# Kernel optimization log

Hardware: AMD Instinct MI355X
Metric: run time of the kernel (lower is better)

The kernel has to match this reference:

```python
import math
import jax, jax.numpy as jnp
import numpy as np

LLM = 4096
QB = 512
SAM = 256
H = W = 64
OUT = 256
HEADS = 4
DH = SAM // HEADS
EPS = 1e-5


def _ln(x, g, b):
    mu = jnp.mean(x, axis=-1, keepdims=True)
    var = jnp.mean(jnp.square(x - mu), axis=-1, keepdims=True)
    return (x - mu) * jax.lax.rsqrt(var + EPS) * g + b


def _conv3x3(x, w):
    # x: (N,C,H,W), w: (O,I,3,3), padding=1
    return jax.lax.conv_general_dilated(
        x, w, window_strides=(1, 1), padding='SAME',
        dimension_numbers=('NCHW', 'OIHW', 'NCHW'))


def setup_inputs() -> dict:
    key = jax.random.key(0)
    ks = jax.random.split(key, 20)
    n = lambda k, sh, s: (jax.random.normal(k, sh, dtype=jnp.float32) * s)
    inp = {
        'image_embed': n(ks[0], (8, SAM, H, W), 1.0),
        'ref_vec': n(ks[1], (8, 32, LLM), 1.0),
        'querybook_slots': n(ks[2], (8, 32, QB), 1.0),
        # parameters (torch Linear layout: (out, in); conv: (O,I,kh,kw))
        'q_proj_w': n(ks[3], (HEADS * DH, LLM), 1.0 / math.sqrt(LLM)),
        'k_proj_w': n(ks[4], (HEADS * DH, SAM, 1, 1), 1.0 / math.sqrt(SAM)),
        'fuser_w1': n(ks[5], (HEADS, HEADS, 3, 3), 1.0 / math.sqrt(HEADS * 9)),
        'fuser_b1': n(ks[6], (HEADS,), 0.01),
        'fuser_w2': n(ks[7], (1, HEADS, 3, 3), 1.0 / math.sqrt(HEADS * 9)),
        'fuser_b2': jnp.full((1,), -1.8, dtype=jnp.float32),
        'qb_proj_w': n(ks[8], (LLM, QB), 1.0 / math.sqrt(QB)),
        'rf_ln_g': jnp.ones((2 * LLM,), jnp.float32),
        'rf_ln_b': jnp.zeros((2 * LLM,), jnp.float32),
        'rf_lin_w': n(ks[9], (LLM, 2 * LLM), 1.0 / math.sqrt(2 * LLM)),
        'rf_lin_b': n(ks[10], (LLM,), 0.01),
        'cf_ln_g': jnp.ones((LLM,), jnp.float32),
        'cf_ln_b': jnp.zeros((LLM,), jnp.float32),
        'cf_w1': n(ks[11], (LLM // 2, LLM), 1.0 / math.sqrt(LLM)),
        'cf_b1': n(ks[12], (LLM // 2,), 0.01),
        'cf_w2': n(ks[13], (1, LLM // 2), 1.0 / math.sqrt(LLM // 2)),
        'cf_b2': n(ks[14], (1,), 0.01),
    }
    return inp


def reference(image_embed, ref_vec, querybook_slots, q_proj_w, k_proj_w,
              fuser_w1, fuser_b1, fuser_w2, fuser_b2, qb_proj_w,
              rf_ln_g, rf_ln_b, rf_lin_w, rf_lin_b,
              cf_ln_g, cf_ln_b, cf_w1, cf_b1, cf_w2, cf_b2):
    B, C, h, w = image_embed.shape
    K = ref_vec.shape[1]
    # querybook projection + ref fuse
    qb = jnp.einsum('bkq,lq->bkl', querybook_slots, qb_proj_w)  # (B,K,LLM)
    cat = jnp.concatenate([ref_vec, qb], axis=-1)               # (B,K,2*LLM)
    fused = jax.nn.silu(jnp.einsum('bkc,lc->bkl', _ln(cat, rf_ln_g, rf_ln_b), rf_lin_w) + rf_lin_b)
    # per-slot query heads
    Q = jnp.einsum('bkl,ol->bko', fused, q_proj_w).reshape(B, K, HEADS, DH)
    # 1x1 conv key map -> (B,HEADS,DH,H,W)
    Kmap = jnp.einsum('bcxy,oc->boxy', image_embed, k_proj_w.reshape(HEADS * DH, SAM))
    Kmap = Kmap.reshape(B, HEADS, DH, h, w)
    # fused contraction over d_head (original materialized (B,K,HEADS,DH,H,W))
    logits_64_heads = jnp.einsum('bkhd,bhdxy->bkhxy', Q, Kmap) / math.sqrt(DH)
    x = logits_64_heads.reshape(B * K, HEADS, h, w)
    x = jax.nn.silu(_conv3x3(x, fuser_w1) + fuser_b1[None, :, None, None])
    logits_64 = _conv3x3(x, fuser_w2) + fuser_b2[None, :, None, None]  # (B*K,1,64,64)
    # bilinear upsample, align_corners=False (half-pixel centers)
    up = jax.image.resize(logits_64, (B * K, 1, OUT, OUT), method='bilinear')
    ref_logits_256 = up.reshape(B, K, OUT, OUT)
    # confidence head
    cfh = jax.nn.silu(jnp.einsum('bkl,ol->bko', _ln(fused, cf_ln_g, cf_ln_b), cf_w1) + cf_b1)
    conf_logits = (jnp.einsum('bko,lo->bkl', cfh, cf_w2) + cf_b2).squeeze(-1)  # (B,K)
    return ref_logits_256, conf_logits
```

## Files before the change

### kernel.cpp

```cpp
#include <hip/hip_runtime.h>

#define EPS 1e-5f

typedef __bf16 bf16_t;
typedef __bf16 bf16x8 __attribute__((ext_vector_type(8)));
typedef __bf16 bf16x4 __attribute__((ext_vector_type(4)));
typedef float f32x4 __attribute__((ext_vector_type(4)));

__device__ __forceinline__ float silu_f(float x) { return x / (1.f + __expf(-x)); }

__device__ __forceinline__ void gll16(const void* g, void* l) {
  __builtin_amdgcn_global_load_lds(
      (const __attribute__((address_space(1))) unsigned int*)g,
      (__attribute__((address_space(3))) unsigned int*)l, 16, 0, 0);
}

__device__ __forceinline__ float block_sum(float v, float* tmp) {
#pragma unroll
  for (int off = 32; off > 0; off >>= 1) v += __shfl_down(v, off);
  __syncthreads();
  if ((threadIdx.x & 63) == 0) tmp[threadIdx.x >> 6] = v;
  __syncthreads();
  return tmp[0] + tmp[1] + tmp[2] + tmp[3];
}

__global__ __launch_bounds__(1024) void gemm_gll(
    const bf16_t* __restrict__ A, const float* __restrict__ B,
    bf16_t* __restrict__ Cpart, int N, int K, int KS) {
  __shared__ bf16_t AsL[2][16384];
  __shared__ float BsL[2][8192];
  const int t = threadIdx.x;
  const int lane = t & 63;
  const int w = t >> 6;
  const int n0 = blockIdx.x * 128;
  const int kbeg = blockIdx.y * KS;
  const int nt = KS >> 6;

  const int arow0 = 16 * w + (lane >> 3);
  const int adch = (lane & 7) ^ (lane >> 3);
  const bf16_t* gA0 = A + (size_t)arow0 * K + kbeg + adch * 8;
  const bf16_t* gA1 = gA0 + (size_t)8 * K;
  const int brow0 = 8 * w + (lane >> 4);
  const int brow1 = brow0 + 4;
  const int bd0 = (lane & 15) ^ (brow0 & 15);
  const int bd1 = (lane & 15) ^ (brow1 & 15);
  const float* gB0 = B + (size_t)(n0 + brow0) * K + kbeg + bd0 * 4;
  const float* gB1 = B + (size_t)(n0 + brow1) * K + kbeg + bd1 * 4;

  f32x4 acc[4][2];
#pragma unroll
  for (int i = 0; i < 4; ++i)
#pragma unroll
    for (int j = 0; j < 2; ++j) acc[i][j] = f32x4{0.f, 0.f, 0.f, 0.f};

  const int wm = (w & 3) * 64;
  const int wn = (w >> 2) * 32;
  const int fr = lane & 15;
  const int kq = (lane >> 4) * 8;

  auto ISSUE = [&](int s, int p) {
    const int koff = s * 64;
    char* ab = (char*)&AsL[p][0] + 2 * w * 1024;
    char* bb = (char*)&BsL[p][0] + 2 * w * 1024;
    gll16(gA0 + koff, ab);
    gll16(gA1 + koff, ab + 1024);
    gll16(gB0 + koff, bb);
    gll16(gB1 + koff, bb + 1024);
  };

  auto COMPUTE = [&](int p) {
    const char* Ab = (const char*)&AsL[p][0];
    const char* Bb = (const char*)&BsL[p][0];
#pragma unroll
    for (int kk = 0; kk < 64; kk += 32) {
      const int col = kk + kq;
      bf16x8 af[4], bg[2];
#pragma unroll
      for (int i = 0; i < 4; ++i) {
        const int ra = wm + 16 * i + fr;
        const int sa = (col >> 3) ^ (ra & 7);
        af[i] = *(const bf16x8*)(Ab + ra * 128 + sa * 16);
      }
#pragma unroll
      for (int j = 0; j < 2; ++j) {
        const int rb = wn + 16 * j + fr;
        const int c0 = col >> 2;
        const int s0 = c0 ^ (rb & 15);
        const int s1 = (c0 + 1) ^ (rb & 15);
        f32x4 u0 = *(const f32x4*)(Bb + rb * 256 + s0 * 16);
        f32x4 u1 = *(const f32x4*)(Bb + rb * 256 + s1 * 16);
        bf16x8 bv;
        bv[0] = (bf16_t)u0[0]; bv[1] = (bf16_t)u0[1];
        bv[2] = (bf16_t)u0[2]; bv[3] = (bf16_t)u0[3];
        bv[4] = (bf16_t)u1[0]; bv[5] = (bf16_t)u1[1];
        bv[6] = (bf16_t)u1[2]; bv[7] = (bf16_t)u1[3];
        bg[j] = bv;
      }
#pragma unroll
      for (int i = 0; i < 4; ++i)
#pragma unroll
        for (int j = 0; j < 2; ++j)
          acc[i][j] = __builtin_amdgcn_mfma_f32_16x16x32_bf16(af[i], bg[j], acc[i][j], 0, 0, 0);
    }
  };

#define SB __builtin_amdgcn_sched_barrier(0);

  ISSUE(0, 0);
  if (nt > 1) ISSUE(1, 1);
  for (int s = 0; s < nt; ++s) {
    const int p = s & 1;
    if (s + 1 < nt) {
      asm volatile("s_waitcnt vmcnt(4)" ::: "memory");
    } else {
      asm volatile("s_waitcnt vmcnt(0)" ::: "memory");
    }
    SB __builtin_amdgcn_s_barrier(); SB
    COMPUTE(p);
    if (s + 2 < nt) {
      asm volatile("s_waitcnt lgkmcnt(0)" ::: "memory");
      SB __builtin_amdgcn_s_barrier(); SB
      ISSUE(s + 2, p);
    }
  }
#undef SB

  bf16_t* Cz = Cpart + (size_t)blockIdx.y * 256 * N;
  const int rh = (lane >> 4) * 4, col = lane & 15;
#pragma unroll
  for (int i = 0; i < 4; ++i)
#pragma unroll
    for (int j = 0; j < 2; ++j)
#pragma unroll
      for (int rr = 0; rr < 4; ++rr)
        Cz[(size_t)(wm + 16 * i + rh + rr) * N + n0 + wn + 16 * j + col] =
            (bf16_t)acc[i][j][rr];
}

__global__ __launch_bounds__(1024) void gemm_wide_s(
    const float* __restrict__ A, const float* __restrict__ B,
    bf16_t* __restrict__ Cpart, int N, int K, int KS) {
  __shared__ bf16_t As[256][72];
  __shared__ bf16_t Bs[128][72];
  const int t = threadIdx.x;
  const int lane = t & 63;
  const int w = t >> 6;
  const int n0 = blockIdx.x * 128;
  const int kbeg = blockIdx.y * KS;
  const int nt = KS >> 6;
  const int ar = t >> 2, ac = (t & 3) * 16;
  const int br = t >> 3, bc = (t & 7) * 8;
  const float* Ap = A + (size_t)ar * K + kbeg + ac;
  const float* Bp = B + (size_t)(n0 + br) * K + kbeg + bc;

  f32x4 acc[4][2];
#pragma unroll
  for (int i = 0; i < 4; ++i)
#pragma unroll
    for (int j = 0; j < 2; ++j) acc[i][j] = f32x4{0.f, 0.f, 0.f, 0.f};

  const int wm = (w & 3) * 64;
  const int wn = (w >> 2) * 32;
  const int fr = lane & 15;
  const int kq = (lane >> 4) * 8;

  for (int s = 0; s < nt; ++s) {
    float4 av[4], bv[2];
#pragma unroll
    for (int i = 0; i < 4; ++i) av[i] = *(const float4*)(Ap + s * 64 + 4 * i);
#pragma unroll
    for (int i = 0; i < 2; ++i) bv[i] = *(const float4*)(Bp + s * 64 + 4 * i);
    __syncthreads();
    {
      bf16x8 wa0, wa1, wb;
      wa0[0] = (bf16_t)av[0].x; wa0[1] = (bf16_t)av[0].y; wa0[2] = (bf16_t)av[0].z; wa0[3] = (bf16_t)av[0].w;
      wa0[4] = (bf16_t)av[1].x; wa0[5] = (bf16_t)av[1].y; wa0[6] = (bf16_t)av[1].z; wa0[7] = (bf16_t)av[1].w;
      wa1[0] = (bf16_t)av[2].x; wa1[1] = (bf16_t)av[2].y; wa1[2] = (bf16_t)av[2].z; wa1[3] = (bf16_t)av[2].w;
      wa1[4] = (bf16_t)av[3].x; wa1[5] = (bf16_t)av[3].y; wa1[6] = (bf16_t)av[3].z; wa1[7] = (bf16_t)av[3].w;
      wb[0] = (bf16_t)bv[0].x; wb[1] = (bf16_t)bv[0].y; wb[2] = (bf16_t)bv[0].z; wb[3] = (bf16_t)bv[0].w;
      wb[4] = (bf16_t)bv[1].x; wb[5] = (bf16_t)bv[1].y; wb[6] = (bf16_t)bv[1].z; wb[7] = (bf16_t)bv[1].w;
      *(bf16x8*)&As[ar][ac] = wa0;
      *(bf16x8*)&As[ar][ac + 8] = wa1;
      *(bf16x8*)&Bs[br][bc] = wb;
    }
    __syncthreads();
#pragma unroll
    for (int kk = 0; kk < 64; kk += 32) {
      bf16x8 af[4], bg[2];
#pragma unroll
      for (int i = 0; i < 4; ++i)
        af[i] = *(const bf16x8*)&As[wm + 16 * i + fr][kk + kq];
#pragma unroll
      for (int j = 0; j < 2; ++j)
        bg[j] = *(const bf16x8*)&Bs[wn + 16 * j + fr][kk + kq];
#pragma unroll
      for (int i = 0; i < 4; ++i)
#pragma unroll
        for (int j = 0; j < 2; ++j)
          acc[i][j] = __builtin_amdgcn_mfma_f32_16x16x32_bf16(af[i], bg[j], acc[i][j], 0, 0, 0);
    }
    __syncthreads();
  }

  bf16_t* Cz = Cpart + (size_t)blockIdx.y * 256 * N;
  const int rh = (lane >> 4) * 4, col = lane & 15;
#pragma unroll
  for (int i = 0; i < 4; ++i)
#pragma unroll
    for (int j = 0; j < 2; ++j)
#pragma unroll
      for (int rr = 0; rr < 4; ++rr)
        Cz[(size_t)(wm + 16 * i + rh + rr) * N + n0 + wn + 16 * j + col] =
            (bf16_t)acc[i][j][rr];
}

__global__ __launch_bounds__(256) void gemm_small(
    const bf16_t* __restrict__ A16, const float* __restrict__ B32, float* __restrict__ Cv,
    int M, int N, int K, int KS, int S) {
  __shared__ bf16_t As[64][72];
  __shared__ bf16_t Bs[64][72];
  const int t = threadIdx.x;
  const int lane = t & 63;
  const int w = t >> 6;
  const int s = blockIdx.z;
  const int n0 = blockIdx.x * 64;
  const int m0 = blockIdx.y * 64;
  const int kbeg = s * KS;

  f32x4 acc[2][2];
#pragma unroll
  for (int i = 0; i < 2; ++i)
#pragma unroll
    for (int j = 0; j < 2; ++j) acc[i][j] = f32x4{0.f, 0.f, 0.f, 0.f};

  const int wm = (w & 1) * 32, wn = (w >> 1) * 32;
  const int fr = lane & 15;
  const int kq = (lane >> 4) * 8;

  for (int k0 = kbeg; k0 < kbeg + KS; k0 += 64) {
    bf16x8 a8[2];
    float4 b4[4];
    {
      const int rr = t >> 2, c8 = (t & 3) * 8;
#pragma unroll
      for (int i = 0; i < 2; ++i)
        a8[i] = *(const bf16x8*)(A16 + (size_t)(m0 + rr) * K + k0 + c8 + 32 * i);
    }
    {
      const int rr = t >> 4, c4 = (t & 15) * 4;
#pragma unroll
      for (int i = 0; i < 4; ++i)
        b4[i] = *(const float4*)(B32 + (size_t)(n0 + rr + 16 * i) * K + k0 + c4);
    }
    __syncthreads();
    {
      const int rr = t >> 2, c8 = (t & 3) * 8;
#pragma unroll
      for (int i = 0; i < 2; ++i) *(bf16x8*)&As[rr][c8 + 32 * i] = a8[i];
    }
    {
      const int rr = t >> 4, c4 = (t & 15) * 4;
#pragma unroll
      for (int i = 0; i < 4; ++i) {
        bf16x4 v = {(bf16_t)b4[i].x, (bf16_t)b4[i].y, (bf16_t)b4[i].z, (bf16_t)b4[i].w};
        *(bf16x4*)&Bs[rr + 16 * i][c4] = v;
      }
    }
    __syncthreads();
#pragma unroll
    for (int kk = 0; kk < 64; kk += 32) {
      bf16x8 af[2], bg[2];
#pragma unroll
      for (int i = 0; i < 2; ++i) {
        af[i] = *(const bf16x8*)&As[wm + 16 * i + fr][kk + kq];
        bg[i] = *(const bf16x8*)&Bs[wn + 16 * i + fr][kk + kq];
      }
#pragma unroll
      for (int i = 0; i < 2; ++i)
#pragma unroll
        for (int j = 0; j < 2; ++j)
          acc[i][j] = __builtin_amdgcn_mfma_f32_16x16x32_bf16(af[i], bg[j], acc[i][j], 0, 0, 0);
    }
    __syncthreads();
  }

  const int rh = (lane >> 4) * 4;
  const int col = lane & 15;
#pragma unroll
  for (int i = 0; i < 2; ++i)
#pragma unroll
    for (int j = 0; j < 2; ++j)
#pragma unroll
      for (int rr = 0; rr < 4; ++rr)
        Cv[(size_t)s * M * N + (size_t)(m0 + wm + 16 * i + rh + rr) * N + n0 + wn + 16 * j + col] =
            acc[i][j][rr];
}

__global__ __launch_bounds__(512) void gemm_attn(
    const float* __restrict__ A, const float* __restrict__ B, bf16_t* __restrict__ C) {
  __shared__ bf16_t As[128][72];
  __shared__ bf16_t Bs[64][72];
  const int t = threadIdx.x;
  const int lane = t & 63;
  const int w = t >> 6;
  const int b = blockIdx.y;
  const int n0 = blockIdx.x * 64;
  const float* Ab = A + (size_t)b * 32768;
  const float* Bb = B + (size_t)b * 1048576;

  f32x4 acc[2][2];
#pragma unroll
  for (int i = 0; i < 2; ++i)
#pragma unroll
    for (int j = 0; j < 2; ++j) acc[i][j] = f32x4{0.f, 0.f, 0.f, 0.f};

  const int wm = (w & 3) * 32;
  const int wn = (w >> 2) * 32;
  const int fr = lane & 15;
  const int kq = (lane >> 4) * 8;

  for (int k0 = 0; k0 < 256; k0 += 64) {
    const int r = t >> 2, c4 = (t & 3) * 16;
    float4 a4[4];
#pragma unroll
    for (int i = 0; i < 4; ++i)
      a4[i] = *(const float4*)(Ab + (size_t)r * 256 + k0 + c4 + 4 * i);
    const int kr = t >> 3, nc = (t & 7) * 8;
    float4 b4[2];
#pragma unroll
    for (int i = 0; i < 2; ++i)
      b4[i] = *(const float4*)(Bb + (size_t)(k0 + kr) * 4096 + n0 + nc + 4 * i);
    __syncthreads();
#pragma unroll
    for (int i = 0; i < 4; ++i) {
      bf16x4 v = {(bf16_t)a4[i].x, (bf16_t)a4[i].y, (bf16_t)a4[i].z, (bf16_t)a4[i].w};
      *(bf16x4*)&As[r][c4 + 4 * i] = v;
    }
#pragma unroll
    for (int i = 0; i < 2; ++i) {
      Bs[nc + 4 * i + 0][kr] = (bf16_t)b4[i].x;
      Bs[nc + 4 * i + 1][kr] = (bf16_t)b4[i].y;
      Bs[nc + 4 * i + 2][kr] = (bf16_t)b4[i].z;
      Bs[nc + 4 * i + 3][kr] = (bf16_t)b4[i].w;
    }
    __syncthreads();
#pragma unroll
    for (int kk = 0; kk < 64; kk += 32) {
      bf16x8 af[2], bg[2];
#pragma unroll
      for (int i = 0; i < 2; ++i) {
        af[i] = *(const bf16x8*)&As[wm + 16 * i + fr][kk + kq];
        bg[i] = *(const bf16x8*)&Bs[wn + 16 * i + fr][kk + kq];
      }
#pragma unroll
      for (int i = 0; i < 2; ++i)
#pragma unroll
        for (int j = 0; j < 2; ++j)
          acc[i][j] = __builtin_amdgcn_mfma_f32_16x16x32_bf16(af[i], bg[j], acc[i][j], 0, 0, 0);
    }
    __syncthreads();
  }

  bf16_t* Cb = C + (size_t)b * 524288;
  const int rh = (lane >> 4) * 4, col = lane & 15;
#pragma unroll
  for (int i = 0; i < 2; ++i)
#pragma unroll
    for (int j = 0; j < 2; ++j)
#pragma unroll
      for (int rr = 0; rr < 4; ++rr)
        Cb[(size_t)(wm + 16 * i + rh + rr) * 4096 + n0 + wn + 16 * j + col] =
            (bf16_t)acc[i][j][rr];
}

template <int SILU_, int BIAS_>
__global__ __launch_bounds__(256) void reduce_b(
    const bf16_t* __restrict__ part, int S, long slice,
    const float* __restrict__ bias, float scale,
    float* __restrict__ outF, bf16_t* __restrict__ outB,
    long nmask, long total8) {
  long i8 = (long)blockIdx.x * 256 + threadIdx.x;
  if (i8 >= total8) return;
  long i = i8 * 8;
  float a[8] = {0.f, 0.f, 0.f, 0.f, 0.f, 0.f, 0.f, 0.f};
  for (int s = 0; s < S; ++s) {
    bf16x8 v = *(const bf16x8*)(part + (size_t)s * slice + i);
#pragma unroll
    for (int j = 0; j < 8; ++j) a[j] += (float)v[j];
  }
#pragma unroll
  for (int j = 0; j < 8; ++j) a[j] *= scale;
  if (BIAS_) {
    const float* bb = bias + (i & nmask);
#pragma unroll
    for (int j = 0; j < 8; ++j) a[j] += bb[j];
  }
  if (SILU_) {
#pragma unroll
    for (int j = 0; j < 8; ++j) a[j] = silu_f(a[j]);
  }
  if (outF) {
    float4 o0 = {a[0], a[1], a[2], a[3]}, o1 = {a[4], a[5], a[6], a[7]};
    *(float4*)(outF + i) = o0;
    *(float4*)(outF + i + 4) = o1;
  }
  if (outB) {
    bf16x8 o;
#pragma unroll
    for (int j = 0; j < 8; ++j) o[j] = (bf16_t)a[j];
    *(bf16x8*)(outB + i) = o;
  }
}

__global__ __launch_bounds__(256) void ln_fuse(
    const float* __restrict__ refv, const bf16_t* __restrict__ partQ, int S,
    const float* __restrict__ g, const float* __restrict__ bta, bf16_t* __restrict__ Y) {
  __shared__ float tmp[4];
  const int row = blockIdx.x;
  const int t = threadIdx.x;
  const long i0 = t * 16;
  float q[16];
#pragma unroll
  for (int j = 0; j < 16; ++j) q[j] = 0.f;
  for (int s = 0; s < S; ++s) {
    const bf16_t* p = partQ + (size_t)s * 1048576 + (size_t)row * 4096 + i0;
    bf16x8 v0 = *(const bf16x8*)(p);
    bf16x8 v1 = *(const bf16x8*)(p + 8);
#pragma unroll
    for (int j = 0; j < 8; ++j) { q[j] += (float)v0[j]; q[8 + j] += (float)v1[j]; }
  }
  const float* xr = refv + (size_t)row * 4096 + i0;
  float r[16];
#pragma unroll
  for (int j = 0; j < 4; ++j) {
    float4 v = *(const float4*)(xr + 4 * j);
    r[4 * j] = v.x; r[4 * j + 1] = v.y; r[4 * j + 2] = v.z; r[4 * j + 3] = v.w;
  }
  float s1 = 0.f, s2 = 0.f;
#pragma unroll
  for (int j = 0; j < 16; ++j) { s1 += r[j] + q[j]; s2 += r[j] * r[j] + q[j] * q[j]; }
  s1 = block_sum(s1, tmp);
  s2 = block_sum(s2, tmp);
  const float mu = s1 / 8192.f;
  const float inv = rsqrtf(s2 / 8192.f - mu * mu + EPS);
  bf16_t* y = Y + (size_t)row * 8192;
  bf16x8 o0, o1;
#pragma unroll
  for (int j = 0; j < 8; ++j) {
    o0[j] = (bf16_t)((r[j] - mu) * inv * g[i0 + j] + bta[i0 + j]);
    o1[j] = (bf16_t)((r[8 + j] - mu) * inv * g[i0 + 8 + j] + bta[i0 + 8 + j]);
  }
  *(bf16x8*)(y + i0) = o0;
  *(bf16x8*)(y + i0 + 8) = o1;
#pragma unroll
  for (int j = 0; j < 8; ++j) {
    o0[j] = (bf16_t)((q[j] - mu) * inv * g[4096 + i0 + j] + bta[4096 + i0 + j]);
    o1[j] = (bf16_t)((q[8 + j] - mu) * inv * g[4096 + i0 + 8 + j] + bta[4096 + i0 + 8 + j]);
  }
  *(bf16x8*)(y + 4096 + i0) = o0;
  *(bf16x8*)(y + 4096 + i0 + 8) = o1;
}

__global__ __launch_bounds__(256) void ln_rows(
    const float* __restrict__ X1, int L1,
    const float* __restrict__ g, const float* __restrict__ bta, bf16_t* __restrict__ Y) {
  __shared__ float tmp[4];
  const int row = blockIdx.x;
  const float* x1 = X1 + (size_t)row * L1;
  float s = 0.f, ss = 0.f;
  for (int i = threadIdx.x * 4; i < L1; i += 1024) {
    float4 v = *(const float4*)(x1 + i);
    s += v.x + v.y + v.z + v.w;
    ss += v.x * v.x + v.y * v.y + v.z * v.z + v.w * v.w;
  }
  s = block_sum(s, tmp);
  ss = block_sum(ss, tmp);
  const float mu = s / (float)L1;
  const float inv = rsqrtf(ss / (float)L1 - mu * mu + EPS);
  bf16_t* y = Y + (size_t)row * L1;
  for (int i = threadIdx.x * 4; i < L1; i += 1024) {
    float4 v = *(const float4*)(x1 + i);
    float4 gv = *(const float4*)(g + i);
    float4 bv = *(const float4*)(bta + i);
    bf16x4 o = {(bf16_t)((v.x - mu) * inv * gv.x + bv.x),
                (bf16_t)((v.y - mu) * inv * gv.y + bv.y),
                (bf16_t)((v.z - mu) * inv * gv.z + bv.z),
                (bf16_t)((v.w - mu) * inv * gv.w + bv.w)};
    *(bf16x4*)(y + i) = o;
  }
}

__global__ __launch_bounds__(256) void qw_fuse(
    const float* __restrict__ part8, const float* __restrict__ kW, float* __restrict__ QW) {
  __shared__ float q[256];
  const int bk = blockIdx.x;
  const int c = threadIdx.x;
  float sq = 0.f;
#pragma unroll
  for (int s = 0; s < 8; ++s) sq += part8[(size_t)s * 65536 + (size_t)bk * 256 + c];
  q[c] = 0.125f * sq;
  __syncthreads();
#pragma unroll
  for (int h = 0; h < 4; ++h) {
    float s = 0.f;
#pragma unroll 8
    for (int d = 0; d < 64; ++d)
      s += q[(h << 6) + d] * kW[(size_t)(((h << 6) + d) << 8) + c];
    QW[((size_t)(bk * 4 + h) << 8) + c] = s;
  }
}

__global__ __launch_bounds__(256) void conv_fused(
    const bf16_t* __restrict__ X, const float* __restrict__ W1,
    const float* __restrict__ B1, const float* __restrict__ W2,
    const float* __restrict__ B2, float* __restrict__ O) {
  __shared__ bf16_t lg[16384];
  __shared__ bf16_t mid[16384];
  __shared__ float lg64[4096];
  __shared__ float wsh[180];
  const int t = threadIdx.x;
  const size_t base = (size_t)blockIdx.x * 16384;
#pragma unroll
  for (int i = 0; i < 8; ++i) {
    int o = (i * 256 + t) * 8;
    *(bf16x8*)&lg[o] = *(const bf16x8*)(X + base + o);
  }
  if (t < 144) wsh[t] = W1[t];
  else if (t < 180) wsh[t] = W2[t - 144];
  __syncthreads();
  const int px0 = (t & 15) * 4, py0 = (t >> 4) * 4;
  {
    float acc1[4][16];
#pragma unroll
    for (int oc = 0; oc < 4; ++oc) {
      float bb = B1[oc];
#pragma unroll
      for (int p = 0; p < 16; ++p) acc1[oc][p] = bb;
    }
#pragma unroll
    for (int c = 0; c < 4; ++c) {
      float p[6][6];
#pragma unroll
      for (int yy = 0; yy < 6; ++yy) {
        int gy = py0 + yy - 1;
#pragma unroll
        for (int xx = 0; xx < 6; ++xx) {
          int gx = px0 + xx - 1;
          p[yy][xx] = ((unsigned)gy < 64u && (unsigned)gx < 64u)
                          ? (float)lg[c * 4096 + gy * 64 + gx] : 0.f;
        }
      }
#pragma unroll
      for (int oc = 0; oc < 4; ++oc) {
        float wr[9];
#pragma unroll
        for (int k = 0; k < 9; ++k) wr[k] = wsh[oc * 36 + c * 9 + k];
#pragma unroll
        for (int y = 0; y < 4; ++y)
#pragma unroll
          for (int x = 0; x < 4; ++x)
            acc1[oc][y * 4 + x] +=
                wr[0] * p[y][x] + wr[1] * p[y][x + 1] + wr[2] * p[y][x + 2]
              + wr[3] * p[y + 1][x] + wr[4] * p[y + 1][x + 1] + wr[5] * p[y + 1][x + 2]
              + wr[6] * p[y + 2][x] + wr[7] * p[y + 2][x + 1] + wr[8] * p[y + 2][x + 2];
      }
    }
#pragma unroll
    for (int oc = 0; oc < 4; ++oc)
#pragma unroll
      for (int y = 0; y < 4; ++y) {
        bf16x4 o;
#pragma unroll
        for (int x = 0; x < 4; ++x) o[x] = (bf16_t)silu_f(acc1[oc][y * 4 + x]);
        *(bf16x4*)&mid[oc * 4096 + (py0 + y) * 64 + px0] = o;
      }
  }
  __syncthreads();
  {
    float acc2[16];
    float bb = B2[0];
#pragma unroll
    for (int p = 0; p < 16; ++p) acc2[p] = bb;
#pragma unroll
    for (int c = 0; c < 4; ++c) {
      float p[6][6];
#pragma unroll
      for (int yy = 0; yy < 6; ++yy) {
        int gy = py0 + yy - 1;
#pragma unroll
        for (int xx = 0; xx < 6; ++xx) {
          int gx = px0 + xx - 1;
          p[yy][xx] = ((unsigned)gy < 64u && (unsigned)gx < 64u)
                          ? (float)mid[c * 4096 + gy * 64 + gx] : 0.f;
        }
      }
      float wr[9];
#pragma unroll
      for (int k = 0; k < 9; ++k) wr[k] = wsh[144 + c * 9 + k];
#pragma unroll
      for (int y = 0; y < 4; ++y)
#pragma unroll
        for (int x = 0; x < 4; ++x)
          acc2[y * 4 + x] +=
              wr[0] * p[y][x] + wr[1] * p[y][x + 1] + wr[2] * p[y][x + 2]
            + wr[3] * p[y + 1][x] + wr[4] * p[y + 1][x + 1] + wr[5] * p[y + 1][x + 2]
            + wr[6] * p[y + 2][x] + wr[7] * p[y + 2][x + 1] + wr[8] * p[y + 2][x + 2];
    }
#pragma unroll
    for (int y = 0; y < 4; ++y)
#pragma unroll
      for (int x = 0; x < 4; ++x) lg64[(py0 + y) * 64 + px0 + x] = acc2[y * 4 + x];
  }
  __syncthreads();
  float* Ob = O + (size_t)blockIdx.x * 65536;
  for (int rr = 0; rr < 64; ++rr) {
    int p4 = rr * 256 + t;
    int oy = p4 >> 6, ox0 = (p4 & 63) * 4;
    float sy = oy * 0.25f - 0.375f;
    int y0 = (int)floorf(sy);
    float wy = sy - (float)y0;
    int y1 = min(y0 + 1, 63); y0 = max(y0, 0);
    const float* r0 = &lg64[y0 * 64];
    const float* r1 = &lg64[y1 * 64];
    float4 o;
#pragma unroll
    for (int q = 0; q < 4; ++q) {
      int ox = ox0 + q;
      float sx = ox * 0.25f - 0.375f;
      int x0 = (int)floorf(sx);
      float wx = sx - (float)x0;
      int x1 = min(x0 + 1, 63); x0 = max(x0, 0);
      float v0 = r0[x0] + wx * (r0[x1] - r0[x0]);
      float v1 = r1[x0] + wx * (r1[x1] - r1[x0]);
      ((float*)&o)[q] = v0 + wy * (v1 - v0);
    }
    *(float4*)(Ob + oy * 256 + ox0) = o;
  }
}

__global__ __launch_bounds__(256) void conf_k(
    const float* __restrict__ cfh, const float* __restrict__ w2,
    const float* __restrict__ b2, float* __restrict__ out) {
  __shared__ float tmp[4];
  const int row = blockIdx.x;
  float s = 0.f;
  for (int i = threadIdx.x; i < 2048; i += 256)
    s += cfh[(size_t)row * 2048 + i] * w2[i];
  s = block_sum(s, tmp);
  if (threadIdx.x == 0) out[row] = s + b2[0];
}

extern "C" void kernel_launch(void* const* d_in, const int* in_sizes, int n_in,
                              void* d_out, int out_size, void* d_ws, size_t ws_size,
                              hipStream_t stream) {
  const float* img    = (const float*)d_in[0];
  const float* refv   = (const float*)d_in[1];
  const float* qs     = (const float*)d_in[2];
  const float* qpw    = (const float*)d_in[3];
  const float* kpw    = (const float*)d_in[4];
  const float* fw1    = (const float*)d_in[5];
  const float* fb1    = (const float*)d_in[6];
  const float* fw2    = (const float*)d_in[7];
  const float* fb2    = (const float*)d_in[8];
  const float* qbw    = (const float*)d_in[9];
  const float* rlg    = (const float*)d_in[10];
  const float* rlb    = (const float*)d_in[11];
  const float* rlw    = (const float*)d_in[12];
  const float* rlbias = (const float*)d_in[13];
  const float* clg    = (const float*)d_in[14];
  const float* clb    = (const float*)d_in[15];
  const float* cw1    = (const float*)d_in[16];
  const float* cb1    = (const float*)d_in[17];
  const float* cw2    = (const float*)d_in[18];
  const float* cb2    = (const float*)d_in[19];
  float* out = (float*)d_out;
  char* W = (char*)d_ws;

  bf16_t* partQ = (bf16_t*)(W + 0);
  bf16_t* partF = (bf16_t*)(W + 0);
  bf16_t* l64hb = (bf16_t*)(W + 0);
  bf16_t* partC = (bf16_t*)(W + 0);
  bf16_t* catln = (bf16_t*)(W + 16777216);
  float*  fus   = (float*)(W + 16777216);
  bf16_t* fusb  = (bf16_t*)(W + 20971520);
  bf16_t* lnf   = (bf16_t*)(W + 20971520);
  float*  part8 = (float*)(W + 23068672);
  float*  QW    = (float*)(W + 25165824);
  float*  cfh   = (float*)(W + 26214400);

  dim3 b256(256);

  gemm_wide_s<<<dim3(32, 8), dim3(1024), 0, stream>>>(qs, qbw, partQ, 4096, 512, 64);
  ln_fuse<<<dim3(256), b256, 0, stream>>>(refv, partQ, 8, rlg, rlb, catln);
  gemm_gll<<<dim3(32, 8), dim3(1024), 0, stream>>>(catln, rlw, partF, 4096, 8192, 1024);
  reduce_b<1, 1><<<dim3(512), b256, 0, stream>>>(
      partF, 8, 1048576L, rlbias, 1.f, fus, fusb, 4095L, 131072L);
  gemm_small<<<dim3(4, 4, 8), b256, 0, stream>>>(fusb, qpw, part8, 256, 256, 4096, 512, 8);
  qw_fuse<<<dim3(256), b256, 0, stream>>>(part8, kpw, QW);
  gemm_attn<<<dim3(64, 8), dim3(512), 0, stream>>>(QW, img, l64hb);
  conv_fused<<<dim3(256), b256, 0, stream>>>(l64hb, fw1, fb1, fw2, fb2, out);
  ln_rows<<<dim3(256), b256, 0, stream>>>(fus, 4096, clg, clb, lnf);
  gemm_gll<<<dim3(16, 8), dim3(1024), 0, stream>>>(lnf, cw1, partC, 2048, 4096, 512);
  reduce_b<1, 1><<<dim3(256), b256, 0, stream>>>(
      partC, 8, 524288L, cb1, 1.f, cfh, nullptr, 2047L, 65536L);
  conf_k<<<dim3(256), b256, 0, stream>>>(cfh, cw2, cb2, out + 16777216);
}
```

Before: 184.7 us.

## Fuse split-K reduction with LayerNorm and confidence head, widen conf GEMM split

The split-K reduction after the fusion linear now also computes the confidence-head LayerNorm, writing the bf16 fused and normalized rows in one kernel. This drops the fp32 intermediate and the separate ln_rows pass. The confidence GEMM's split-K factor goes from 8 to 16 for more blocks. Its reduction, bias, SiLU and final dot product are fused into one kernel, removing two launches and the fp32 cfh buffer. The cost is reading twice as many partial sums in the last reduction.

```diff
diff --git a/kernel.cpp b/kernel.cpp
--- a/kernel.cpp
+++ b/kernel.cpp
@@ -373,43 +373,49 @@
             (bf16_t)acc[i][j][rr];
 }
 
-template <int SILU_, int BIAS_>
-__global__ __launch_bounds__(256) void reduce_b(
-    const bf16_t* __restrict__ part, int S, long slice,
-    const float* __restrict__ bias, float scale,
-    float* __restrict__ outF, bf16_t* __restrict__ outB,
-    long nmask, long total8) {
-  long i8 = (long)blockIdx.x * 256 + threadIdx.x;
-  if (i8 >= total8) return;
-  long i = i8 * 8;
-  float a[8] = {0.f, 0.f, 0.f, 0.f, 0.f, 0.f, 0.f, 0.f};
+__global__ __launch_bounds__(256) void red_ln(
+    const bf16_t* __restrict__ partF, int S,
+    const float* __restrict__ bias,
+    const float* __restrict__ g, const float* __restrict__ bta,
+    bf16_t* __restrict__ fusb, bf16_t* __restrict__ lnf) {
+  __shared__ float tmp[4];
+  const int row = blockIdx.x;
+  const int t = threadIdx.x;
+  const long i0 = t * 16;
+  float a[16];
+#pragma unroll
+  for (int j = 0; j < 16; ++j) a[j] = 0.f;
   for (int s = 0; s < S; ++s) {
-    bf16x8 v = *(const bf16x8*)(part + (size_t)s * slice + i);
-#pragma unroll
-    for (int j = 0; j < 8; ++j) a[j] += (float)v[j];
-  }
-#pragma unroll
-  for (int j = 0; j < 8; ++j) a[j] *= scale;
-  if (BIAS_) {
-    const float* bb = bias + (i & nmask);
-#pragma unroll
-    for (int j = 0; j < 8; ++j) a[j] += bb[j];
-  }
-  if (SILU_) {
-#pragma unroll
-    for (int j = 0; j < 8; ++j) a[j] = silu_f(a[j]);
-  }
-  if (outF) {
-    float4 o0 = {a[0], a[1], a[2], a[3]}, o1 = {a[4], a[5], a[6], a[7]};
-    *(float4*)(outF + i) = o0;
-    *(float4*)(outF + i + 4) = o1;
-  }
-  if (outB) {
-    bf16x8 o;
-#pragma unroll
-    for (int j = 0; j < 8; ++j) o[j] = (bf16_t)a[j];
-    *(bf16x8*)(outB + i) = o;
-  }
+    const bf16_t* p = partF + (size_t)s * 1048576 + (size_t)row * 4096 + i0;
+    bf16x8 v0 = *(const bf16x8*)(p);
+    bf16x8 v1 = *(const bf16x8*)(p + 8);
+#pragma unroll
+    for (int j = 0; j < 8; ++j) { a[j] += (float)v0[j]; a[8 + j] += (float)v1[j]; }
+  }
+#pragma unroll
+  for (int j = 0; j < 16; ++j) a[j] = silu_f(a[j] + bias[i0 + j]);
+  {
+    bf16x8 o0, o1;
+#pragma unroll
+    for (int j = 0; j < 8; ++j) { o0[j] = (bf16_t)a[j]; o1[j] = (bf16_t)a[8 + j]; }
+    *(bf16x8*)(fusb + (size_t)row * 4096 + i0) = o0;
+    *(bf16x8*)(fusb + (size_t)row * 4096 + i0 + 8) = o1;
+  }
+  float s1 = 0.f, s2 = 0.f;
+#pragma unroll
+  for (int j = 0; j < 16; ++j) { s1 += a[j]; s2 += a[j] * a[j]; }
+  s1 = block_sum(s1, tmp);
+  s2 = block_sum(s2, tmp);
+  const float mu = s1 / 4096.f;
+  const float inv = rsqrtf(s2 / 4096.f - mu * mu + EPS);
+  bf16x8 o0, o1;
+#pragma unroll
+  for (int j = 0; j < 8; ++j) {
+    o0[j] = (bf16_t)((a[j] - mu) * inv * g[i0 + j] + bta[i0 + j]);
+    o1[j] = (bf16_t)((a[8 + j] - mu) * inv * g[i0 + 8 + j] + bta[i0 + 8 + j]);
+  }
+  *(bf16x8*)(lnf + (size_t)row * 4096 + i0) = o0;
+  *(bf16x8*)(lnf + (size_t)row * 4096 + i0 + 8) = o1;
 }
 
 __global__ __launch_bounds__(256) void ln_fuse(
@@ -459,35 +465,6 @@
   }
   *(bf16x8*)(y + 4096 + i0) = o0;
   *(bf16x8*)(y + 4096 + i0 + 8) = o1;
-}
-
-__global__ __launch_bounds__(256) void ln_rows(
-    const float* __restrict__ X1, int L1,
-    const float* __restrict__ g, const float* __restrict__ bta, bf16_t* __restrict__ Y) {
-  __shared__ float tmp[4];
-  const int row = blockIdx.x;
-  const float* x1 = X1 + (size_t)row * L1;
-  float s = 0.f, ss = 0.f;
-  for (int i = threadIdx.x * 4; i < L1; i += 1024) {
-    float4 v = *(const float4*)(x1 + i);
-    s += v.x + v.y + v.z + v.w;
-    ss += v.x * v.x + v.y * v.y + v.z * v.z + v.w * v.w;
-  }
-  s = block_sum(s, tmp);
-  ss = block_sum(ss, tmp);
-  const float mu = s / (float)L1;
-  const float inv = rsqrtf(ss / (float)L1 - mu * mu + EPS);
-  bf16_t* y = Y + (size_t)row * L1;
-  for (int i = threadIdx.x * 4; i < L1; i += 1024) {
-    float4 v = *(const float4*)(x1 + i);
-    float4 gv = *(const float4*)(g + i);
-    float4 bv = *(const float4*)(bta + i);
-    bf16x4 o = {(bf16_t)((v.x - mu) * inv * gv.x + bv.x),
-                (bf16_t)((v.y - mu) * inv * gv.y + bv.y),
-                (bf16_t)((v.z - mu) * inv * gv.z + bv.z),
-                (bf16_t)((v.w - mu) * inv * gv.w + bv.w)};
-    *(bf16x4*)(y + i) = o;
-  }
 }
 
 __global__ __launch_bounds__(256) void qw_fuse(
@@ -638,16 +615,27 @@
   }
 }
 
-__global__ __launch_bounds__(256) void conf_k(
-    const float* __restrict__ cfh, const float* __restrict__ w2,
+__global__ __launch_bounds__(256) void conf_fuse(
+    const bf16_t* __restrict__ partC, int S,
+    const float* __restrict__ cb1, const float* __restrict__ w2,
     const float* __restrict__ b2, float* __restrict__ out) {
   __shared__ float tmp[4];
   const int row = blockIdx.x;
-  float s = 0.f;
-  for (int i = threadIdx.x; i < 2048; i += 256)
-    s += cfh[(size_t)row * 2048 + i] * w2[i];
-  s = block_sum(s, tmp);
-  if (threadIdx.x == 0) out[row] = s + b2[0];
+  const int t = threadIdx.x;
+  const long i0 = t * 8;
+  float a[8];
+#pragma unroll
+  for (int j = 0; j < 8; ++j) a[j] = 0.f;
+  for (int s = 0; s < S; ++s) {
+    bf16x8 v = *(const bf16x8*)(partC + (size_t)s * 524288 + (size_t)row * 2048 + i0);
+#pragma unroll
+    for (int j = 0; j < 8; ++j) a[j] += (float)v[j];
+  }
+  float dot = 0.f;
+#pragma unroll
+  for (int j = 0; j < 8; ++j) dot += silu_f(a[j] + cb1[i0 + j]) * w2[i0 + j];
+  dot = block_sum(dot, tmp);
+  if (t == 0) out[row] = dot + b2[0];
 }
 
 extern "C" void kernel_launch(void* const* d_in, const int* in_sizes, int n_in,
@@ -681,27 +669,21 @@
   bf16_t* l64hb = (bf16_t*)(W + 0);
   bf16_t* partC = (bf16_t*)(W + 0);
   bf16_t* catln = (bf16_t*)(W + 16777216);
-  float*  fus   = (float*)(W + 16777216);
   bf16_t* fusb  = (bf16_t*)(W + 20971520);
-  bf16_t* lnf   = (bf16_t*)(W + 20971520);
-  float*  part8 = (float*)(W + 23068672);
-  float*  QW    = (float*)(W + 25165824);
-  float*  cfh   = (float*)(W + 26214400);
+  bf16_t* lnf   = (bf16_t*)(W + 23068672);
+  float*  part8 = (float*)(W + 25165824);
+  float*  QW    = (float*)(W + 27262976);
 
   dim3 b256(256);
 
   gemm_wide_s<<<dim3(32, 8), dim3(1024), 0, stream>>>(qs, qbw, partQ, 4096, 512, 64);
   ln_fuse<<<dim3(256), b256, 0, stream>>>(refv, partQ, 8, rlg, rlb, catln);
   gemm_gll<<<dim3(32, 8), dim3(1024), 0, stream>>>(catln, rlw, partF, 4096, 8192, 1024);
-  reduce_b<1, 1><<<dim3(512), b256, 0, stream>>>(
-      partF, 8, 1048576L, rlbias, 1.f, fus, fusb, 4095L, 131072L);
+  red_ln<<<dim3(256), b256, 0, stream>>>(partF, 8, rlbias, clg, clb, fusb, lnf);
   gemm_small<<<dim3(4, 4, 8), b256, 0, stream>>>(fusb, qpw, part8, 256, 256, 4096, 512, 8);
   qw_fuse<<<dim3(256), b256, 0, stream>>>(part8, kpw, QW);
   gemm_attn<<<dim3(64, 8), dim3(512), 0, stream>>>(QW, img, l64hb);
   conv_fused<<<dim3(256), b256, 0, stream>>>(l64hb, fw1, fb1, fw2, fb2, out);
-  ln_rows<<<dim3(256), b256, 0, stream>>>(fus, 4096, clg, clb, lnf);
-  gemm_gll<<<dim3(16, 8), dim3(1024), 0, stream>>>(lnf, cw1, partC, 2048, 4096, 512);
-  reduce_b<1, 1><<<dim3(256), b256, 0, stream>>>(
-      partC, 8, 524288L, cb1, 1.f, cfh, nullptr, 2047L, 65536L);
-  conf_k<<<dim3(256), b256, 0, stream>>>(cfh, cw2, cb2, out + 16777216);
-}
+  gemm_gll<<<dim3(16, 16), dim3(1024), 0, stream>>>(lnf, cw1, partC, 2048, 4096, 256);
+  conf_fuse<<<dim3(256), b256, 0, stream>>>(partC, 16, cb1, cw2, cb2, out + 16777216);
+}
```

Result: faster. 178.0 us (-3.6%).
